# Performance work log

Measured on AMD Instinct MI355X. Metric: run time of the kernel, lower is better.

Reference implementation:

```python
import jax, jax.numpy as jnp
import numpy as np

NUM_GROUPS = 32
NUM_HEADS = 4
EPS = 1e-5


def setup_inputs() -> dict:
    key = jax.random.key(0)
    ks = jax.random.split(key, 6)
    B, C, H, W = 16, 512, 32, 32
    x = jax.random.normal(ks[0], (B, C, H, W), dtype=jnp.float32)
    gn_w = jax.random.normal(ks[1], (C,), dtype=jnp.float32) * 0.02 + 1.0
    gn_b = jax.random.normal(ks[2], (C,), dtype=jnp.float32) * 0.02
    # 1x1 convs are channel matmuls: store as [out_ch, in_ch]
    w_qkv = jax.random.normal(ks[3], (3 * C, C), dtype=jnp.float32) * (C ** -0.5)
    w_out = jax.random.normal(ks[4], (C, C), dtype=jnp.float32) * (C ** -0.5)
    b_out = jax.random.normal(ks[5], (C,), dtype=jnp.float32) * 0.02
    return {"x": x, "gn_w": gn_w, "gn_b": gn_b, "w_qkv": w_qkv, "w_out": w_out, "b_out": b_out}


def _group_norm(x, w, b):
    B, C, H, W = x.shape
    g = NUM_GROUPS
    xg = x.reshape(B, g, C // g, H, W)
    mean = xg.mean(axis=(2, 3, 4), keepdims=True)
    var = xg.var(axis=(2, 3, 4), keepdims=True)
    xn = ((xg - mean) * jax.lax.rsqrt(var + EPS)).reshape(B, C, H, W)
    return xn * w[None, :, None, None] + b[None, :, None, None]


def reference(x, gn_w, gn_b, w_qkv, w_out, b_out):
    B, C, H, W = x.shape
    h = NUM_HEADS
    d = C // h
    scale = d ** -0.5
    xn = _group_norm(x, gn_w, gn_b)
    # 1x1 conv QKV projection: [3C, C] @ channels
    qkv = jnp.einsum('oc,bchw->bohw', w_qkv, xn)
    q, k, v = jnp.split(qkv, 3, axis=1)
    # [B, h, d, HW]
    q = q.reshape(B, h, d, H * W)
    k = k.reshape(B, h, d, H * W)
    v = v.reshape(B, h, d, H * W)
    scores = jnp.einsum('bhdi,bhdj->bhij', q, k) * scale
    probs = jax.nn.softmax(scores, axis=-1)
    out = jnp.einsum('bhij,bhdj->bhdi', probs, v)
    out = out.reshape(B, C, H, W)
    out = jnp.einsum('oc,bchw->bohw', w_out, out) + b_out[None, :, None, None]
    return out + x
```

## Files before the change

### kernel.cpp

```cpp
#include <hip/hip_runtime.h>
#include <hip/hip_bf16.h>

#define B_    16
#define C_    512
#define HW_   1024
#define G_    32
#define CPG_  16
#define NH_   4
#define D_    128
#define EPS_  1e-5f
#define SCALE_ 0.08838834764831845f
#define SCALE_L2E_ 0.1275174306f

typedef short bf16x8 __attribute__((ext_vector_type(8)));
typedef short bf16x4 __attribute__((ext_vector_type(4)));
typedef float f32x4  __attribute__((ext_vector_type(4)));

typedef __attribute__((address_space(3))) unsigned int lds_u32_t;
typedef const __attribute__((address_space(1))) unsigned int glb_u32_t;

__device__ __forceinline__ bf16x8 ld8(const __hip_bfloat16* p) {
    return *reinterpret_cast<const bf16x8*>(p);
}
__device__ __forceinline__ void gload16(const __hip_bfloat16* g, __hip_bfloat16* l) {
    __builtin_amdgcn_global_load_lds((glb_u32_t*)(const void*)g,
                                     (lds_u32_t*)(void*)l, 16, 0, 0);
}
__device__ __forceinline__ unsigned pack_bf2(float a, float b) {
    union { __hip_bfloat16 h; unsigned short u; } ua, ub;
    ua.h = __float2bfloat16(a); ub.h = __float2bfloat16(b);
    return ((unsigned)ub.u << 16) | (unsigned)ua.u;
}

__global__ __launch_bounds__(256) void convert_w(
    const float* __restrict__ wqkv, const float* __restrict__ wout,
    __hip_bfloat16* __restrict__ wqkv_bf, __hip_bfloat16* __restrict__ wout_bf) {
    const int i = (blockIdx.x * 256 + threadIdx.x) * 4;
    if (i < 3 * C_ * C_) {
        float4 v = *reinterpret_cast<const float4*>(wqkv + i);
        union { bf16x4 s; __hip_bfloat16 h[4]; } u;
        u.h[0] = __float2bfloat16(v.x); u.h[1] = __float2bfloat16(v.y);
        u.h[2] = __float2bfloat16(v.z); u.h[3] = __float2bfloat16(v.w);
        *reinterpret_cast<bf16x4*>(wqkv_bf + i) = u.s;
    }
    if (i < C_ * C_) {
        float4 v = *reinterpret_cast<const float4*>(wout + i);
        union { bf16x4 s; __hip_bfloat16 h[4]; } u;
        u.h[0] = __float2bfloat16(v.x); u.h[1] = __float2bfloat16(v.y);
        u.h[2] = __float2bfloat16(v.z); u.h[3] = __float2bfloat16(v.w);
        *reinterpret_cast<bf16x4*>(wout_bf + i) = u.s;
    }
}

__global__ __launch_bounds__(256) void gn_kernel(
    const float* __restrict__ x, const float* __restrict__ gnw,
    const float* __restrict__ gnb, __hip_bfloat16* __restrict__ xn_t) {
    const int b = blockIdx.x >> 5;
    const int g = blockIdx.x & 31;
    const float* xp = x + ((size_t)(b * C_ + g * CPG_)) * HW_;

    float s = 0.f, s2 = 0.f;
    const float4* xv = reinterpret_cast<const float4*>(xp);
    #pragma unroll
    for (int t = 0; t < 16; ++t) {
        float4 v = xv[threadIdx.x + t * 256];
        s  += v.x + v.y + v.z + v.w;
        s2 += v.x * v.x + v.y * v.y + v.z * v.z + v.w * v.w;
    }
    #pragma unroll
    for (int off = 32; off > 0; off >>= 1) {
        s  += __shfl_down(s,  off, 64);
        s2 += __shfl_down(s2, off, 64);
    }
    __shared__ float ss[4], ss2[4];
    if ((threadIdx.x & 63) == 0) { ss[threadIdx.x >> 6] = s; ss2[threadIdx.x >> 6] = s2; }
    __syncthreads();
    s = ss[0] + ss[1] + ss[2] + ss[3];
    s2 = ss2[0] + ss2[1] + ss2[2] + ss2[3];
    const float mean = s * (1.f / 16384.f);
    const float inv  = rsqrtf(fmaxf(s2 * (1.f / 16384.f) - mean * mean, 0.f) + EPS_);

    float a[16], bb[16];
    #pragma unroll
    for (int cc = 0; cc < 16; ++cc) {
        float w = gnw[g * CPG_ + cc];
        a[cc] = inv * w;
        bb[cc] = gnb[g * CPG_ + cc] - mean * inv * w;
    }

    for (int hw = threadIdx.x; hw < HW_; hw += 256) {
        union { bf16x8 v; __hip_bfloat16 h[8]; } u0, u1;
        #pragma unroll
        for (int cc = 0; cc < 8; ++cc)
            u0.h[cc] = __float2bfloat16(xp[cc * HW_ + hw] * a[cc] + bb[cc]);
        #pragma unroll
        for (int cc = 8; cc < 16; ++cc)
            u1.h[cc - 8] = __float2bfloat16(xp[cc * HW_ + hw] * a[cc] + bb[cc]);
        __hip_bfloat16* dst = xn_t + ((size_t)(b * HW_ + hw)) * C_ + g * CPG_;
        *reinterpret_cast<bf16x8*>(dst) = u0.v;
        *reinterpret_cast<bf16x8*>(dst + 8) = u1.v;
    }
}

#define PH_(r, s) (((r) * 8 + ((s) ^ ((r) & 7))) * 8)

__global__ __launch_bounds__(256, 2) void qkv_gemm(
    const __hip_bfloat16* __restrict__ W, const __hip_bfloat16* __restrict__ xn_t,
    __hip_bfloat16* __restrict__ q_t, __hip_bfloat16* __restrict__ k_t,
    __hip_bfloat16* __restrict__ v_s) {
    const int id   = blockIdx.x;
    const int virt = (id & 7) * 192 + (id >> 3);
    const int ot   = virt % 12;
    const int rest = virt / 12;
    const int itl  = rest & 7;
    const int b    = rest >> 3;
    const int o0 = ot * 128, i0 = itl * 128;

    const int t = threadIdx.x;
    const int w = t >> 6, lane = t & 63, l16 = lane & 15, lg = lane >> 4;
    const int wr = w >> 1, wc = w & 1;
    const __hip_bfloat16* xb = xn_t + (size_t)b * HW_ * C_;

    __shared__ __align__(16) __hip_bfloat16 Ab[2][128 * 64];
    __shared__ __align__(16) __hip_bfloat16 Bb[2][128 * 64];

    const int r8  = lane >> 3;
    const int ssl = (lane & 7) ^ r8;
    auto issue = [&](int kk, int bi) {
        #pragma unroll
        for (int j = 0; j < 4; ++j) {
            const int row = w * 32 + j * 8 + r8;
            gload16(W  + (size_t)(o0 + row) * C_ + kk + ssl * 8, &Ab[bi][(w * 32 + j * 8) * 64]);
            gload16(xb + (size_t)(i0 + row) * C_ + kk + ssl * 8, &Bb[bi][(w * 32 + j * 8) * 64]);
        }
    };

    f32x4 acc[4][4];
    const f32x4 z = {0.f, 0.f, 0.f, 0.f};
    #pragma unroll
    for (int m = 0; m < 4; ++m)
        #pragma unroll
        for (int n = 0; n < 4; ++n) acc[m][n] = z;

    issue(0, 0);
    for (int ks = 0; ks < 8; ++ks) {
        __syncthreads();
        if (ks < 7) issue((ks + 1) * 64, (ks + 1) & 1);
        const __hip_bfloat16* Ac = Ab[ks & 1];
        const __hip_bfloat16* Bc = Bb[ks & 1];
        #pragma unroll
        for (int kks = 0; kks < 2; ++kks) {
            bf16x8 af[4], bfr[4];
            #pragma unroll
            for (int m = 0; m < 4; ++m)
                af[m] = ld8(&Ac[PH_(wr * 64 + m * 16 + l16, kks * 4 + lg)]);
            #pragma unroll
            for (int n = 0; n < 4; ++n)
                bfr[n] = ld8(&Bc[PH_(wc * 64 + n * 16 + l16, kks * 4 + lg)]);
            if (ot < 8) {
                #pragma unroll
                for (int m = 0; m < 4; ++m)
                    #pragma unroll
                    for (int n = 0; n < 4; ++n)
                        acc[m][n] = __builtin_amdgcn_mfma_f32_16x16x32_bf16(bfr[n], af[m], acc[m][n], 0, 0, 0);
            } else {
                #pragma unroll
                for (int m = 0; m < 4; ++m)
                    #pragma unroll
                    for (int n = 0; n < 4; ++n)
                        acc[m][n] = __builtin_amdgcn_mfma_f32_16x16x32_bf16(af[m], bfr[n], acc[m][n], 0, 0, 0);
            }
        }
    }

    if (ot < 4) {
        const int hd = ot;
        __hip_bfloat16* base = q_t + (size_t)(b * NH_ + hd) * HW_ * D_;
        const int dd = wr * 64 + l16;
        #pragma unroll
        for (int m = 0; m < 4; ++m)
            #pragma unroll
            for (int n = 0; n < 4; ++n)
                #pragma unroll
                for (int r = 0; r < 4; ++r) {
                    const int i = i0 + wc * 64 + n * 16 + lg * 4 + r;
                    base[(size_t)i * D_ + dd + m * 16] = __float2bfloat16(acc[m][n][r] * SCALE_L2E_);
                }
    } else if (ot < 8) {
        const int hd = ot - 4;
        __hip_bfloat16* base = k_t + (size_t)(b * NH_ + hd) * HW_ * D_;
        const int dd = wr * 64 + l16;
        #pragma unroll
        for (int m = 0; m < 4; ++m)
            #pragma unroll
            for (int n = 0; n < 4; ++n)
                #pragma unroll
                for (int r = 0; r < 4; ++r) {
                    const int i = i0 + wc * 64 + n * 16 + lg * 4 + r;
                    base[(size_t)i * D_ + dd + m * 16] = __float2bfloat16(acc[m][n][r]);
                }
    } else {
        const int hd = ot - 8;
        __hip_bfloat16* base = v_s + (size_t)(b * NH_ + hd) * D_ * HW_;
        #pragma unroll
        for (int m = 0; m < 4; ++m)
            #pragma unroll
            for (int r = 0; r < 4; ++r) {
                const int dd = wr * 64 + m * 16 + lg * 4 + r;
                #pragma unroll
                for (int n = 0; n < 4; ++n) {
                    const int i = i0 + wc * 64 + n * 16 + l16;
                    base[(size_t)dd * HW_ + i] = __float2bfloat16(acc[m][n][r]);
                }
            }
    }
}

__global__ __launch_bounds__(512, 4) void attn_kernel(
    const __hip_bfloat16* __restrict__ q_t, const __hip_bfloat16* __restrict__ k_t,
    const __hip_bfloat16* __restrict__ v_s, __hip_bfloat16* __restrict__ at) {
    const int id  = blockIdx.x;
    const int xcd = id & 7;
    const int q8  = id >> 3;
    const int hb  = xcd * 8 + (q8 >> 3);
    const int it  = q8 & 7;
    const int h   = hb & 3;
    const int b   = hb >> 2;

    const int t = threadIdx.x;
    const int w  = t >> 6;
    const int lane = t & 63;
    const int l16 = lane & 15, lg = lane >> 4;
    const size_t bh = (size_t)b * NH_ + h;
    const __hip_bfloat16* qp = q_t + bh * HW_ * D_;
    const __hip_bfloat16* kp = k_t + bh * HW_ * D_;
    const __hip_bfloat16* vp = v_s + bh * D_ * HW_;
    const int i0 = it * 128 + w * 16;

    __shared__ __align__(16) __hip_bfloat16 kbuf[64 * 128];
    __shared__ __align__(16) __hip_bfloat16 vbuf[128 * 64];
    __shared__ __align__(16) __hip_bfloat16 P2[8][16][72];

    #define KPHYS(row, c) (((row) * 16 + ((c) ^ ((row) & 7))) * 8)
    #define VPHYS(row, c) (((row) * 8  + ((c) ^ ((row) & 7))) * 8)

    const int krow = t >> 3, kc = t & 7;
    const int vrow = t >> 2, vc = t & 3;

    bf16x8 kreg0, kreg1, vreg0, vreg1;
    auto issue_loads = [&](int j0) {
        kreg0 = ld8(kp + (size_t)(j0 + krow) * D_ + kc * 8);
        kreg1 = ld8(kp + (size_t)(j0 + krow) * D_ + (kc + 8) * 8);
        vreg0 = ld8(vp + (size_t)vrow * HW_ + j0 + vc * 8);
        vreg1 = ld8(vp + (size_t)vrow * HW_ + j0 + (vc + 4) * 8);
    };

    bf16x8 aq[4];
    #pragma unroll
    for (int kd = 0; kd < 4; ++kd)
        aq[kd] = ld8(qp + (size_t)(i0 + l16) * D_ + kd * 32 + lg * 8);

    f32x4 accO[8];
    const f32x4 z = {0.f, 0.f, 0.f, 0.f};
    #pragma unroll
    for (int tt = 0; tt < 8; ++tt) accO[tt] = z;
    float m_run = -INFINITY;
    float l_run = 0.f;

    issue_loads(0);

    for (int jb = 0; jb < 16; ++jb) {
        __syncthreads();
        *reinterpret_cast<bf16x8*>(&kbuf[KPHYS(krow, kc)])     = kreg0;
        *reinterpret_cast<bf16x8*>(&kbuf[KPHYS(krow, kc + 8)]) = kreg1;
        *reinterpret_cast<bf16x8*>(&vbuf[VPHYS(vrow, vc)])     = vreg0;
        *reinterpret_cast<bf16x8*>(&vbuf[VPHYS(vrow, vc + 4)]) = vreg1;
        __syncthreads();
        if (jb < 15) issue_loads((jb + 1) * 64);

        f32x4 st[4];
        #pragma unroll
        for (int jt = 0; jt < 4; ++jt) st[jt] = z;
        #pragma unroll
        for (int jt = 0; jt < 4; ++jt)
            #pragma unroll
            for (int kd = 0; kd < 4; ++kd) {
                bf16x8 bk = ld8(&kbuf[KPHYS(jt * 16 + l16, kd * 4 + lg)]);
                st[jt] = __builtin_amdgcn_mfma_f32_16x16x32_bf16(bk, aq[kd], st[jt], 0, 0, 0);
            }

        float mx = fmaxf(fmaxf(st[0][0], st[0][1]), fmaxf(st[0][2], st[0][3]));
        #pragma unroll
        for (int jt = 1; jt < 4; ++jt)
            mx = fmaxf(mx, fmaxf(fmaxf(st[jt][0], st[jt][1]), fmaxf(st[jt][2], st[jt][3])));
        mx = fmaxf(mx, __shfl_xor(mx, 16, 64));
        mx = fmaxf(mx, __shfl_xor(mx, 32, 64));

        if (__any(mx > m_run + 8.f)) {
            float mnew = fmaxf(m_run, mx);
            float alpha = exp2f(m_run - mnew);
            m_run = mnew;
            l_run *= alpha;
            float al[4];
            #pragma unroll
            for (int r = 0; r < 4; ++r) al[r] = __shfl(alpha, lg * 4 + r, 64);
            const f32x4 a4 = {al[0], al[1], al[2], al[3]};
            #pragma unroll
            for (int tt = 0; tt < 8; ++tt) accO[tt] *= a4;
        }

        float sum = 0.f;
        #pragma unroll
        for (int jt = 0; jt < 4; ++jt) {
            float p0 = exp2f(st[jt][0] - m_run), p1 = exp2f(st[jt][1] - m_run);
            float p2 = exp2f(st[jt][2] - m_run), p3 = exp2f(st[jt][3] - m_run);
            sum += (p0 + p1) + (p2 + p3);
            uint2 uu = { pack_bf2(p0, p1), pack_bf2(p2, p3) };
            *reinterpret_cast<uint2*>(&P2[w][l16][jt * 16 + lg * 4]) = uu;
        }
        sum += __shfl_xor(sum, 16, 64);
        sum += __shfl_xor(sum, 32, 64);
        l_run += sum;

        #pragma unroll
        for (int ks = 0; ks < 2; ++ks) {
            bf16x8 pa = ld8(&P2[w][l16][ks * 32 + lg * 8]);
            #pragma unroll
            for (int dt = 0; dt < 8; ++dt) {
                bf16x8 bv = ld8(&vbuf[VPHYS(dt * 16 + l16, ks * 4 + lg)]);
                accO[dt] = __builtin_amdgcn_mfma_f32_16x16x32_bf16(pa, bv, accO[dt], 0, 0, 0);
            }
        }
    }

    const float linv = 1.f / l_run;
    float rl[4];
    #pragma unroll
    for (int r = 0; r < 4; ++r) rl[r] = __shfl(linv, lg * 4 + r, 64);
    #pragma unroll
    for (int r = 0; r < 4; ++r) {
        const int i = i0 + lg * 4 + r;
        #pragma unroll
        for (int dt = 0; dt < 8; ++dt)
            at[((size_t)b * HW_ + i) * C_ + h * D_ + dt * 16 + l16] =
                __float2bfloat16(accO[dt][r] * rl[r]);
    }
    #undef KPHYS
    #undef VPHYS
}

__global__ __launch_bounds__(256, 2) void out_gemm(
    const __hip_bfloat16* __restrict__ W, const __hip_bfloat16* __restrict__ at,
    const float* __restrict__ b_out, const float* __restrict__ x,
    float* __restrict__ out) {
    const int id   = blockIdx.x;
    const int virt = (id & 7) * 64 + (id >> 3);
    const int ot   = virt & 3;
    const int rest = virt >> 2;
    const int itl  = rest & 7;
    const int b    = rest >> 3;
    const int o0 = ot * 128, i0 = itl * 128;

    const int t = threadIdx.x;
    const int w = t >> 6, lane = t & 63, l16 = lane & 15, lg = lane >> 4;
    const int wr = w >> 1, wc = w & 1;
    const __hip_bfloat16* ab = at + (size_t)b * HW_ * C_;

    __shared__ __align__(16) __hip_bfloat16 Ab[2][128 * 64];
    __shared__ __align__(16) __hip_bfloat16 Bb[2][128 * 64];

    const int r8  = lane >> 3;
    const int ssl = (lane & 7) ^ r8;
    auto issue = [&](int kk, int bi) {
        #pragma unroll
        for (int j = 0; j < 4; ++j) {
            const int row = w * 32 + j * 8 + r8;
            gload16(W  + (size_t)(o0 + row) * C_ + kk + ssl * 8, &Ab[bi][(w * 32 + j * 8) * 64]);
            gload16(ab + (size_t)(i0 + row) * C_ + kk + ssl * 8, &Bb[bi][(w * 32 + j * 8) * 64]);
        }
    };

    f32x4 acc[4][4];
    const f32x4 z = {0.f, 0.f, 0.f, 0.f};
    #pragma unroll
    for (int m = 0; m < 4; ++m)
        #pragma unroll
        for (int n = 0; n < 4; ++n) acc[m][n] = z;

    issue(0, 0);
    for (int ks = 0; ks < 8; ++ks) {
        __syncthreads();
        if (ks < 7) issue((ks + 1) * 64, (ks + 1) & 1);
        const __hip_bfloat16* Ac = Ab[ks & 1];
        const __hip_bfloat16* Bc = Bb[ks & 1];
        #pragma unroll
        for (int kks = 0; kks < 2; ++kks) {
            bf16x8 af[4], bfr[4];
            #pragma unroll
            for (int m = 0; m < 4; ++m)
                af[m] = ld8(&Ac[PH_(wr * 64 + m * 16 + l16, kks * 4 + lg)]);
            #pragma unroll
            for (int n = 0; n < 4; ++n)
                bfr[n] = ld8(&Bc[PH_(wc * 64 + n * 16 + l16, kks * 4 + lg)]);
            #pragma unroll
            for (int m = 0; m < 4; ++m)
                #pragma unroll
                for (int n = 0; n < 4; ++n)
                    acc[m][n] = __builtin_amdgcn_mfma_f32_16x16x32_bf16(af[m], bfr[n], acc[m][n], 0, 0, 0);
        }
    }

    #pragma unroll
    for (int m = 0; m < 4; ++m)
        #pragma unroll
        for (int r = 0; r < 4; ++r) {
            const int o = o0 + wr * 64 + m * 16 + lg * 4 + r;
            const float bo = b_out[o];
            #pragma unroll
            for (int n = 0; n < 4; ++n) {
                const int i = i0 + wc * 64 + n * 16 + l16;
                const size_t idx = ((size_t)(b * C_ + o)) * HW_ + i;
                out[idx] = acc[m][n][r] + bo + x[idx];
            }
        }
}

extern "C" void kernel_launch(void* const* d_in, const int* in_sizes, int n_in,
                              void* d_out, int out_size, void* d_ws, size_t ws_size,
                              hipStream_t stream) {
    (void)in_sizes; (void)n_in; (void)out_size; (void)ws_size;
    const float* x     = (const float*)d_in[0];
    const float* gn_w  = (const float*)d_in[1];
    const float* gn_b  = (const float*)d_in[2];
    const float* w_qkv = (const float*)d_in[3];
    const float* w_out = (const float*)d_in[4];
    const float* b_out = (const float*)d_in[5];
    float* out = (float*)d_out;

    char* ws = (char*)d_ws;
    size_t off = 0;
    auto alloc = [&](size_t bytes) { void* p = ws + off; off += (bytes + 255) & ~255ULL; return p; };
    __hip_bfloat16* wqkv_bf = (__hip_bfloat16*)alloc((size_t)3 * C_ * C_ * 2);
    __hip_bfloat16* wout_bf = (__hip_bfloat16*)alloc((size_t)C_ * C_ * 2);
    __hip_bfloat16* xn_t    = (__hip_bfloat16*)alloc((size_t)B_ * HW_ * C_ * 2);
    __hip_bfloat16* q_t     = (__hip_bfloat16*)alloc((size_t)B_ * HW_ * C_ * 2);
    __hip_bfloat16* k_t     = (__hip_bfloat16*)alloc((size_t)B_ * HW_ * C_ * 2);
    __hip_bfloat16* v_s     = (__hip_bfloat16*)alloc((size_t)B_ * HW_ * C_ * 2);
    __hip_bfloat16* at      = xn_t;

    convert_w<<<768, 256, 0, stream>>>(w_qkv, w_out, wqkv_bf, wout_bf);
    gn_kernel<<<512, 256, 0, stream>>>(x, gn_w, gn_b, xn_t);
    qkv_gemm<<<1536, 256, 0, stream>>>(wqkv_bf, xn_t, q_t, k_t, v_s);
    attn_kernel<<<512, 512, 0, stream>>>(q_t, k_t, v_s, at);
    out_gemm<<<512, 256, 0, stream>>>(wout_bf, at, b_out, x, out);
}
```

Before: 130.4 us.

## Rewrite attention with 32x32 MFMA, register-resident P and async LDS double buffering

The attention kernel moves from 16x16x32 to 32x32x16 bf16 MFMA tiles, with 4 waves of 256 threads each owning 32 query rows. Probabilities are packed with v_cvt_pk_bf16 and rearranged with permlane32_swap, so they stay in registers instead of round-tripping through LDS. K/V tiles are double-buffered and loaded straight into LDS with global_load_lds, which removes one barrier per iteration and the register staging. The output goes through an LDS transpose so it can be written with 16-byte stores. In exchange each thread holds more registers and fewer threads are resident per block.

```diff
diff --git a/kernel.cpp b/kernel.cpp
--- a/kernel.cpp
+++ b/kernel.cpp
@@ -15,6 +15,7 @@
 typedef short bf16x8 __attribute__((ext_vector_type(8)));
 typedef short bf16x4 __attribute__((ext_vector_type(4)));
 typedef float f32x4  __attribute__((ext_vector_type(4)));
+typedef float f32x16 __attribute__((ext_vector_type(16)));
 
 typedef __attribute__((address_space(3))) unsigned int lds_u32_t;
 typedef const __attribute__((address_space(1))) unsigned int glb_u32_t;
@@ -26,10 +27,10 @@
     __builtin_amdgcn_global_load_lds((glb_u32_t*)(const void*)g,
                                      (lds_u32_t*)(void*)l, 16, 0, 0);
 }
-__device__ __forceinline__ unsigned pack_bf2(float a, float b) {
-    union { __hip_bfloat16 h; unsigned short u; } ua, ub;
-    ua.h = __float2bfloat16(a); ub.h = __float2bfloat16(b);
-    return ((unsigned)ub.u << 16) | (unsigned)ua.u;
+__device__ __forceinline__ unsigned cvtpk_bf16(float lo, float hi) {
+    unsigned r;
+    asm("v_cvt_pk_bf16_f32 %0, %1, %2" : "=v"(r) : "v"(lo), "v"(hi));
+    return r;
 }
 
 __global__ __launch_bounds__(256) void convert_w(
@@ -216,7 +217,7 @@
     }
 }
 
-__global__ __launch_bounds__(512, 4) void attn_kernel(
+__global__ __launch_bounds__(256, 2) void attn_kernel(
     const __hip_bfloat16* __restrict__ q_t, const __hip_bfloat16* __restrict__ k_t,
     const __hip_bfloat16* __restrict__ v_s, __hip_bfloat16* __restrict__ at) {
     const int id  = blockIdx.x;
@@ -230,70 +231,72 @@
     const int t = threadIdx.x;
     const int w  = t >> 6;
     const int lane = t & 63;
-    const int l16 = lane & 15, lg = lane >> 4;
+    const int l32 = lane & 31;
+    const int hi  = lane >> 5;
     const size_t bh = (size_t)b * NH_ + h;
     const __hip_bfloat16* qp = q_t + bh * HW_ * D_;
     const __hip_bfloat16* kp = k_t + bh * HW_ * D_;
     const __hip_bfloat16* vp = v_s + bh * D_ * HW_;
-    const int i0 = it * 128 + w * 16;
-
-    __shared__ __align__(16) __hip_bfloat16 kbuf[64 * 128];
-    __shared__ __align__(16) __hip_bfloat16 vbuf[128 * 64];
-    __shared__ __align__(16) __hip_bfloat16 P2[8][16][72];
+    const int i0 = it * 128 + w * 32;
+
+    __shared__ __align__(16) char smem[2][32768];
 
     #define KPHYS(row, c) (((row) * 16 + ((c) ^ ((row) & 7))) * 8)
     #define VPHYS(row, c) (((row) * 8  + ((c) ^ ((row) & 7))) * 8)
 
-    const int krow = t >> 3, kc = t & 7;
-    const int vrow = t >> 2, vc = t & 3;
-
-    bf16x8 kreg0, kreg1, vreg0, vreg1;
-    auto issue_loads = [&](int j0) {
-        kreg0 = ld8(kp + (size_t)(j0 + krow) * D_ + kc * 8);
-        kreg1 = ld8(kp + (size_t)(j0 + krow) * D_ + (kc + 8) * 8);
-        vreg0 = ld8(vp + (size_t)vrow * HW_ + j0 + vc * 8);
-        vreg1 = ld8(vp + (size_t)vrow * HW_ + j0 + (vc + 4) * 8);
+    const int kri = lane >> 4, ksl = lane & 15;
+    const int vri = lane >> 3, vsl = lane & 7;
+    auto issue = [&](int j0, int bi) {
+        __hip_bfloat16* kb = (__hip_bfloat16*)(smem[bi]);
+        __hip_bfloat16* vb = (__hip_bfloat16*)(smem[bi] + 16384);
+        #pragma unroll
+        for (int i = 0; i < 4; ++i) {
+            const int kr = w * 16 + i * 4 + kri;
+            gload16(kp + (size_t)(j0 + kr) * D_ + ((ksl ^ (kr & 7)) * 8),
+                    kb + (w * 16 + i * 4) * 128);
+            const int vr = w * 32 + i * 8 + vri;
+            gload16(vp + (size_t)vr * HW_ + j0 + ((vsl ^ (vr & 7)) * 8),
+                    vb + (w * 32 + i * 8) * 64);
+        }
     };
 
-    bf16x8 aq[4];
-    #pragma unroll
-    for (int kd = 0; kd < 4; ++kd)
-        aq[kd] = ld8(qp + (size_t)(i0 + l16) * D_ + kd * 32 + lg * 8);
-
-    f32x4 accO[8];
-    const f32x4 z = {0.f, 0.f, 0.f, 0.f};
-    #pragma unroll
-    for (int tt = 0; tt < 8; ++tt) accO[tt] = z;
+    bf16x8 aq[8];
+    #pragma unroll
+    for (int ds = 0; ds < 8; ++ds)
+        aq[ds] = ld8(qp + (size_t)(i0 + l32) * D_ + ds * 16 + hi * 8);
+
+    f32x16 accO[4];
+    #pragma unroll
+    for (int d = 0; d < 4; ++d)
+        #pragma unroll
+        for (int e = 0; e < 16; ++e) accO[d][e] = 0.f;
     float m_run = -INFINITY;
     float l_run = 0.f;
 
-    issue_loads(0);
+    issue(0, 0);
 
     for (int jb = 0; jb < 16; ++jb) {
         __syncthreads();
-        *reinterpret_cast<bf16x8*>(&kbuf[KPHYS(krow, kc)])     = kreg0;
-        *reinterpret_cast<bf16x8*>(&kbuf[KPHYS(krow, kc + 8)]) = kreg1;
-        *reinterpret_cast<bf16x8*>(&vbuf[VPHYS(vrow, vc)])     = vreg0;
-        *reinterpret_cast<bf16x8*>(&vbuf[VPHYS(vrow, vc + 4)]) = vreg1;
-        __syncthreads();
-        if (jb < 15) issue_loads((jb + 1) * 64);
-
-        f32x4 st[4];
-        #pragma unroll
-        for (int jt = 0; jt < 4; ++jt) st[jt] = z;
-        #pragma unroll
-        for (int jt = 0; jt < 4; ++jt)
-            #pragma unroll
-            for (int kd = 0; kd < 4; ++kd) {
-                bf16x8 bk = ld8(&kbuf[KPHYS(jt * 16 + l16, kd * 4 + lg)]);
-                st[jt] = __builtin_amdgcn_mfma_f32_16x16x32_bf16(bk, aq[kd], st[jt], 0, 0, 0);
-            }
-
-        float mx = fmaxf(fmaxf(st[0][0], st[0][1]), fmaxf(st[0][2], st[0][3]));
-        #pragma unroll
-        for (int jt = 1; jt < 4; ++jt)
-            mx = fmaxf(mx, fmaxf(fmaxf(st[jt][0], st[jt][1]), fmaxf(st[jt][2], st[jt][3])));
-        mx = fmaxf(mx, __shfl_xor(mx, 16, 64));
+        if (jb < 15) issue((jb + 1) * 64, (jb + 1) & 1);
+        const __hip_bfloat16* kb = (const __hip_bfloat16*)(smem[jb & 1]);
+        const __hip_bfloat16* vb = (const __hip_bfloat16*)(smem[jb & 1] + 16384);
+
+        f32x16 st0, st1;
+        #pragma unroll
+        for (int e = 0; e < 16; ++e) { st0[e] = 0.f; st1[e] = 0.f; }
+        #pragma unroll
+        for (int ds = 0; ds < 8; ++ds) {
+            bf16x8 kf0 = ld8(&kb[KPHYS(l32,      ds * 2 + hi)]);
+            bf16x8 kf1 = ld8(&kb[KPHYS(32 + l32, ds * 2 + hi)]);
+            st0 = __builtin_amdgcn_mfma_f32_32x32x16_bf16(kf0, aq[ds], st0, 0, 0, 0);
+            st1 = __builtin_amdgcn_mfma_f32_32x32x16_bf16(kf1, aq[ds], st1, 0, 0, 0);
+        }
+
+        float mx = fmaxf(st0[0], st0[1]);
+        #pragma unroll
+        for (int r = 2; r < 16; ++r) mx = fmaxf(mx, st0[r]);
+        #pragma unroll
+        for (int r = 0; r < 16; ++r) mx = fmaxf(mx, st1[r]);
         mx = fmaxf(mx, __shfl_xor(mx, 32, 64));
 
         if (__any(mx > m_run + 8.f)) {
@@ -301,49 +304,62 @@
             float alpha = exp2f(m_run - mnew);
             m_run = mnew;
             l_run *= alpha;
-            float al[4];
-            #pragma unroll
-            for (int r = 0; r < 4; ++r) al[r] = __shfl(alpha, lg * 4 + r, 64);
-            const f32x4 a4 = {al[0], al[1], al[2], al[3]};
-            #pragma unroll
-            for (int tt = 0; tt < 8; ++tt) accO[tt] *= a4;
-        }
-
+            #pragma unroll
+            for (int d = 0; d < 4; ++d)
+                #pragma unroll
+                for (int e = 0; e < 16; ++e) accO[d][e] *= alpha;
+        }
+
+        float p0[16], p1[16];
         float sum = 0.f;
         #pragma unroll
-        for (int jt = 0; jt < 4; ++jt) {
-            float p0 = exp2f(st[jt][0] - m_run), p1 = exp2f(st[jt][1] - m_run);
-            float p2 = exp2f(st[jt][2] - m_run), p3 = exp2f(st[jt][3] - m_run);
-            sum += (p0 + p1) + (p2 + p3);
-            uint2 uu = { pack_bf2(p0, p1), pack_bf2(p2, p3) };
-            *reinterpret_cast<uint2*>(&P2[w][l16][jt * 16 + lg * 4]) = uu;
-        }
-        sum += __shfl_xor(sum, 16, 64);
+        for (int r = 0; r < 16; ++r) { p0[r] = exp2f(st0[r] - m_run); sum += p0[r]; }
+        #pragma unroll
+        for (int r = 0; r < 16; ++r) { p1[r] = exp2f(st1[r] - m_run); sum += p1[r]; }
         sum += __shfl_xor(sum, 32, 64);
         l_run += sum;
 
-        #pragma unroll
-        for (int ks = 0; ks < 2; ++ks) {
-            bf16x8 pa = ld8(&P2[w][l16][ks * 32 + lg * 8]);
-            #pragma unroll
-            for (int dt = 0; dt < 8; ++dt) {
-                bf16x8 bv = ld8(&vbuf[VPHYS(dt * 16 + l16, ks * 4 + lg)]);
-                accO[dt] = __builtin_amdgcn_mfma_f32_16x16x32_bf16(pa, bv, accO[dt], 0, 0, 0);
-            }
-        }
-    }
-
+        #define PV_STEP(PARR, KS) do {                                          \
+            const int g0 = ((KS) & 1) * 2;                                      \
+            unsigned a0 = cvtpk_bf16(PARR[g0 * 4 + 0], PARR[g0 * 4 + 1]);       \
+            unsigned a1 = cvtpk_bf16(PARR[g0 * 4 + 2], PARR[g0 * 4 + 3]);       \
+            unsigned b0 = cvtpk_bf16(PARR[g0 * 4 + 4], PARR[g0 * 4 + 5]);       \
+            unsigned b1 = cvtpk_bf16(PARR[g0 * 4 + 6], PARR[g0 * 4 + 7]);       \
+            asm volatile("v_permlane32_swap_b32 %0, %1" : "+v"(a0), "+v"(b0));  \
+            asm volatile("v_permlane32_swap_b32 %0, %1" : "+v"(a1), "+v"(b1));  \
+            union { unsigned u[4]; bf16x8 v; } pf;                              \
+            pf.u[0] = a0; pf.u[1] = a1; pf.u[2] = b0; pf.u[3] = b1;             \
+            _Pragma("unroll")                                                   \
+            for (int dt = 0; dt < 4; ++dt) {                                    \
+                bf16x8 vf = ld8(&vb[VPHYS(dt * 32 + l32, (KS) * 2 + hi)]);      \
+                accO[dt] = __builtin_amdgcn_mfma_f32_32x32x16_bf16(              \
+                    vf, pf.v, accO[dt], 0, 0, 0);                               \
+            }                                                                   \
+        } while (0)
+        PV_STEP(p0, 0);
+        PV_STEP(p0, 1);
+        PV_STEP(p1, 2);
+        PV_STEP(p1, 3);
+        #undef PV_STEP
+    }
+
+    __syncthreads();
     const float linv = 1.f / l_run;
-    float rl[4];
-    #pragma unroll
-    for (int r = 0; r < 4; ++r) rl[r] = __shfl(linv, lg * 4 + r, 64);
-    #pragma unroll
-    for (int r = 0; r < 4; ++r) {
-        const int i = i0 + lg * 4 + r;
-        #pragma unroll
-        for (int dt = 0; dt < 8; ++dt)
-            at[((size_t)b * HW_ + i) * C_ + h * D_ + dt * 16 + l16] =
-                __float2bfloat16(accO[dt][r] * rl[r]);
+    __hip_bfloat16* Ep = (__hip_bfloat16*)smem + w * (32 * 132);
+    #pragma unroll
+    for (int dt = 0; dt < 4; ++dt)
+        #pragma unroll
+        for (int r = 0; r < 16; ++r) {
+            const int d = dt * 32 + (r & 3) + 4 * hi + 8 * (r >> 2);
+            Ep[l32 * 132 + d] = __float2bfloat16(accO[dt][r] * linv);
+        }
+    __hip_bfloat16* ob = at + ((size_t)b * HW_ + i0) * C_ + h * D_;
+    #pragma unroll
+    for (int rr = 0; rr < 8; ++rr) {
+        const int row = rr * 4 + (lane >> 4);
+        const int col = (lane & 15) * 8;
+        bf16x8 vv = ld8(&Ep[row * 132 + col]);
+        *reinterpret_cast<bf16x8*>(ob + (size_t)row * C_ + col) = vv;
     }
     #undef KPHYS
     #undef VPHYS
@@ -451,6 +467,6 @@
     convert_w<<<768, 256, 0, stream>>>(w_qkv, w_out, wqkv_bf, wout_bf);
     gn_kernel<<<512, 256, 0, stream>>>(x, gn_w, gn_b, xn_t);
     qkv_gemm<<<1536, 256, 0, stream>>>(wqkv_bf, xn_t, q_t, k_t, v_s);
-    attn_kernel<<<512, 512, 0, stream>>>(q_t, k_t, v_s, at);
+    attn_kernel<<<512, 256, 0, stream>>>(q_t, k_t, v_s, at);
     out_gemm<<<512, 256, 0, stream>>>(wout_bf, at, b_out, x, out);
 }
```

Result: faster. 125.0 us (-4.2%).
